# Kernel optimization log

Measured on AMD Instinct MI355X. Metric: run time of the kernel, lower is better.

Reference implementation:

```python
import jax, jax.numpy as jnp
import numpy as np

K = 16      # n_sample neighbors
L = 2       # stacked PT blocks
D = 128     # in_dim
H = 128     # hidden_dim = out_dim = vector_dim
EPS = 1e-5


def _bn(x, g, b, axes):
    # batch-norm with batch statistics (train-mode MinkowskiBatchNorm / BN1d / BN2d)
    m = jnp.mean(x, axes, keepdims=True)
    v = jnp.var(x, axes, keepdims=True)
    return (x - m) * jax.lax.rsqrt(v + EPS) * g + b


def setup_inputs():
    key = jax.random.key(0)
    ks = jax.random.split(key, 16)
    B, Nper = 2, 8192
    coords = jax.random.randint(ks[0], (B, Nper, 3), 0, 200, dtype=jnp.int32)
    feats = jax.random.normal(ks[1], (B * Nper, D), dtype=jnp.float32)
    w = lambda k, s: jax.random.normal(k, s, dtype=jnp.float32) * 0.1
    return {
        'coords': coords, 'feats': feats,
        'W_top': w(ks[2], (L, D, H)),
        'bn_top_g': jnp.ones((L, H)), 'bn_top_b': jnp.zeros((L, H)),
        'W_phi': w(ks[3], (L, H, H)),
        'W_psi': w(ks[4], (L, H, H)),
        'W_alpha': w(ks[5], (L, H, H)),
        'W_d1': w(ks[6], (L, 3, H)), 'b_d1': jnp.zeros((L, H)),
        'bn_d1_g': jnp.ones((L, H)), 'bn_d1_b': jnp.zeros((L, H)),
        'W_d2': w(ks[7], (L, H, H)), 'b_d2': jnp.zeros((L, H)),
        'bn_d2_g': jnp.ones((L, H)), 'bn_d2_b': jnp.zeros((L, H)),
        'W_g1': w(ks[8], (L, H, H)), 'b_g1': jnp.zeros((L, H)),
        'bn_g1_g': jnp.ones((L, H)), 'bn_g1_b': jnp.zeros((L, H)),
        'W_g2': w(ks[9], (L, H, H)), 'b_g2': jnp.zeros((L, H)),
        'bn_g2_g': jnp.ones((L, H)), 'bn_g2_b': jnp.zeros((L, H)),
        'W_down': w(ks[10], (L, H, D)),
        'bn_down_g': jnp.ones((L, D)), 'bn_down_b': jnp.zeros((L, D)),
    }


def _knn(coords):
    # cube_query with USE_KNN=True: per-scene KNN grouping (self included)
    cf = coords.astype(jnp.float32)

    def one(c):  # c: (Nper, 3)
        d2 = jnp.sum((c[:, None, :] - c[None, :, :]) ** 2, -1)  # (Nper, Nper)
        _, idx = jax.lax.top_k(-d2, K)
        return idx

    idx = jax.vmap(one)(cf)                      # (B, Nper, K) per-scene indices
    nbr = jax.vmap(lambda c, i: c[i])(cf, idx)   # (B, Nper, K, 3) grouped coords
    rel = nbr - cf[:, :, None, :]                # relative xyz (pose input)
    B, Nper = coords.shape[0], coords.shape[1]
    gidx = (idx + (jnp.arange(B, dtype=idx.dtype) * Nper)[:, None, None]).reshape(-1, K)
    return rel.reshape(-1, K, 3), gidx           # (N,K,3), (N,K) global indices


def reference(coords, feats, W_top, bn_top_g, bn_top_b, W_phi, W_psi, W_alpha,
              W_d1, b_d1, bn_d1_g, bn_d1_b, W_d2, b_d2, bn_d2_g, bn_d2_b,
              W_g1, b_g1, bn_g1_g, bn_g1_b, W_g2, b_g2, bn_g2_g, bn_g2_b,
              W_down, bn_down_g, bn_down_b):
    rel, gidx = _knn(coords)
    f = feats
    for l in range(L):
        h = _bn(f @ W_top[l], bn_top_g[l], bn_top_b[l], 0)  # linear_top (1x1 conv + BN)
        # delta: pointwise MLP 3 -> H -> H on relative xyz (position encoding)
        pose = jax.nn.relu(_bn(rel @ W_d1[l] + b_d1[l], bn_d1_g[l], bn_d1_b[l], (0, 1)))
        pose = _bn(pose @ W_d2[l] + b_d2[l], bn_d2_g[l], bn_d2_b[l], (0, 1))  # (N,K,H)
        q = h @ W_phi[l]               # (N, H)
        kk = (h @ W_psi[l])[gidx]      # neighbor keys   (N, K, H)
        v = (h @ W_alpha[l])[gidx]     # neighbor values (N, K, H)
        # gamma: pointwise MLP on (phi - psi + pose), vector attention logits
        a = q[:, None, :] - kk + pose
        a = jax.nn.relu(_bn(a @ W_g1[l] + b_g1[l], bn_g1_g[l], bn_g1_b[l], (0, 1)))
        a = _bn(a @ W_g2[l] + b_g2[l], bn_g2_g[l], bn_g2_b[l], (0, 1))
        attn = jax.nn.softmax(a, axis=1)          # per-channel softmax over K neighbors
        y = jnp.sum(attn * (v + pose), axis=1)    # (N, H) vector-attention aggregation
        y = _bn(y @ W_down[l], bn_down_g[l], bn_down_b[l], 0)  # linear_down + BN
        f = y + f                                  # residual
    return f
```

## Files before the change

kernel.cpp:

```cpp
#include <hip/hip_runtime.h>

using u16 = unsigned short;
using u32 = unsigned int;
using u64 = unsigned long long;

#define NPTS   16384
#define NPER   8192
#define KNN    16
#define NKROWS (NPTS*KNN)
#define HD     128
#define CAP    208
#define NSLOT  16

typedef _Float16 half8 __attribute__((ext_vector_type(8)));
typedef float    floatx4 __attribute__((ext_vector_type(4)));

__device__ __forceinline__ u16  f2h(float f){ _Float16 h=(_Float16)f; return __builtin_bit_cast(u16,h); }
__device__ __forceinline__ float h2f(u16 u){ return (float)__builtin_bit_cast(_Float16,u); }
__device__ __forceinline__ u32 umin32(u32 a,u32 b){ return a<b?a:b; }
__device__ __forceinline__ u32 mbcnt64(u64 m){
    return __builtin_amdgcn_mbcnt_hi((u32)(m>>32), __builtin_amdgcn_mbcnt_lo((u32)m,0));
}

__global__ __launch_bounds__(256) void pack_coords(const int* __restrict__ coords, u32* __restrict__ pc){
    int i = blockIdx.x*256 + threadIdx.x;
    pc[i] = (u32)coords[3*i] | ((u32)coords[3*i+1]<<8) | ((u32)coords[3*i+2]<<16);
}

struct WPtrs { const float* p[8]; };
__global__ __launch_bounds__(256) void prep_weights(WPtrs wp, u16* __restrict__ wt){
    int idx = blockIdx.x*256 + threadIdx.x;
    int t = idx>>15, rem = idx&32767;
    int l = rem>>14, e = rem&16383;
    int n = e>>7, k = e&127;
    wt[idx] = f2h(wp.p[t][l*16384 + k*128 + n]);
}

__global__ __launch_bounds__(512) void knn3(const u32* __restrict__ pc, int* __restrict__ idx_g,
                                            float* __restrict__ rel, u64* __restrict__ sM){
    __shared__ u32 sc[NPER];
    __shared__ u32 buf[8][CAP];
    __shared__ u64 red[9];
    int tid = threadIdx.x;
    int wave = tid>>6, lane = tid&63;
    int scene = blockIdx.x >> 10;
    int q = (blockIdx.x & 1023)*8 + wave;

    const uint4* s4 = (const uint4*)(pc + scene*NPER);
#pragma unroll
    for (int i=0;i<4;i++) ((uint4*)sc)[tid + i*512] = s4[tid + i*512];
    if (tid<9) red[tid]=0;
    if (lane<16) buf[wave][lane]=0xFFFFFFFFu;
    __syncthreads();

    u32 qp = sc[q];
    int qx=(int)(qp&255), qy=(int)((qp>>8)&255), qz=(int)((qp>>16)&255);
    u32 thresh = 0xFFFFFFFFu;
    u32 cnt = 16;

    auto tighten = [&](){
        u32 v0 = (lane      < (int)cnt) ? buf[wave][lane]      : 0xFFFFFFFFu;
        u32 v1 = (lane+64   < (int)cnt) ? buf[wave][lane+64]   : 0xFFFFFFFFu;
        u32 v2 = (lane+128  < (int)cnt) ? buf[wave][lane+128]  : 0xFFFFFFFFu;
        u32 v3 = (lane+192  < (int)cnt) ? buf[wave][lane+192]  : 0xFFFFFFFFu;
        u32 T = 0;
#pragma unroll
        for (int b=29;b>=0;b--){
            u32 Tt = T | (1u<<b);
            int c = __popcll(__ballot(v0<Tt)) + __popcll(__ballot(v1<Tt))
                  + __popcll(__ballot(v2<Tt)) + __popcll(__ballot(v3<Tt));
            if (c < 16) T = Tt;
        }
        u64 m0=__ballot(v0<=T), m1=__ballot(v1<=T), m2=__ballot(v2<=T), m3=__ballot(v3<=T);
        u32 b0=(u32)__popcll(m0), b1=(u32)__popcll(m1), b2=(u32)__popcll(m2);
        if (v0<=T) buf[wave][mbcnt64(m0)]=v0;
        if (v1<=T) buf[wave][b0+mbcnt64(m1)]=v1;
        if (v2<=T) buf[wave][b0+b1+mbcnt64(m2)]=v2;
        if (v3<=T) buf[wave][b0+b1+b2+mbcnt64(m3)]=v3;
        cnt = 16;
        thresh = T;
    };

    int lane2 = lane*2;
    uint2 p2 = ((const uint2*)sc)[lane];
    for (int t=0;t<64;t++){
        uint2 cur = p2;
        if (t<63) p2 = ((const uint2*)sc)[(t+1)*64+lane];
        int base = t*128 + lane2;
        u32 pa = cur.x;
        int dx0=(int)(pa&255)-qx, dy0=(int)((pa>>8)&255)-qy, dz0=(int)((pa>>16)&255)-qz;
        u32 d2_0 = (u32)(__mul24(dx0,dx0)+__mul24(dy0,dy0)+__mul24(dz0,dz0));
        u32 key0 = (d2_0<<13) + (u32)base;
        u32 pb = cur.y;
        int dx1=(int)(pb&255)-qx, dy1=(int)((pb>>8)&255)-qy, dz1=(int)((pb>>16)&255)-qz;
        u32 d2_1 = (u32)(__mul24(dx1,dx1)+__mul24(dy1,dy1)+__mul24(dz1,dz1));
        u32 key1 = (d2_1<<13) + (u32)(base+1);
        u64 m0 = __ballot(key0 < thresh);
        if (m0){
            u32 lt = mbcnt64(m0);
            if (key0 < thresh) buf[wave][cnt + lt] = key0;
            cnt += (u32)__popcll(m0);
            if (cnt > CAP-64) tighten();
        }
        u64 m1 = __ballot(key1 < thresh);
        if (m1){
            u32 lt = mbcnt64(m1);
            if (key1 < thresh) buf[wave][cnt + lt] = key1;
            cnt += (u32)__popcll(m1);
            if (cnt > CAP-64) tighten();
        }
    }
    tighten();

    {
        u32 myk = buf[wave][lane & 15];
        u32 rank = 0;
#pragma unroll
        for (int j=0;j<16;j++){ u32 o = buf[wave][j]; rank += (o < myk) ? 1u : 0u; }
        if (lane < 16) buf[wave][rank] = myk;
    }

    int n = scene*NPER + q;
    u32 key = buf[wave][lane & 15];
    int dx=0,dy=0,dz=0;
    if (lane<16){
        int j = (int)(key & 8191u);
        idx_g[(size_t)n*KNN + lane] = scene*NPER + j;
        u32 p = sc[j];
        dx=(int)(p&255)-qx; dy=(int)((p>>8)&255)-qy; dz=(int)((p>>16)&255)-qz;
        size_t ro = ((size_t)n*KNN+lane)*3;
        rel[ro]=(float)dx; rel[ro+1]=(float)dy; rel[ro+2]=(float)dz;
    }
    int arr[9] = {dx,dy,dz, dx*dx,dy*dy,dz*dz, dx*dy,dx*dz,dy*dz};
#pragma unroll
    for (int o=32;o>=1;o>>=1)
#pragma unroll
        for (int j=0;j<9;j++) arr[j] += __shfl_xor(arr[j], o, 64);
    if (lane==0)
#pragma unroll
        for (int j=0;j<9;j++) atomicAdd(&red[j], (u64)(long long)arr[j]);
    __syncthreads();
    if (tid<9) atomicAdd(&sM[tid], red[tid]);
}

__global__ __launch_bounds__(256) void finalize_d1(const u64* __restrict__ sM, const float* __restrict__ W_d1,
        const float* __restrict__ b_d1, const float* __restrict__ g, const float* __restrict__ beta,
        float* __restrict__ A, float* __restrict__ C){
    int tid=threadIdx.x; int l=tid>>7, c=tid&127;
    double s0=(double)(long long)sM[0], s1=(double)(long long)sM[1], s2=(double)(long long)sM[2];
    double m00=(double)(long long)sM[3], m11=(double)(long long)sM[4], m22=(double)(long long)sM[5];
    double m01=(double)(long long)sM[6], m02=(double)(long long)sM[7], m12=(double)(long long)sM[8];
    double w0=W_d1[l*384+c], w1=W_d1[l*384+128+c], w2=W_d1[l*384+256+c];
    double b =b_d1[l*128+c];
    double S = s0*w0+s1*w1+s2*w2;
    double Q = m00*w0*w0+m11*w1*w1+m22*w2*w2 + 2.0*(m01*w0*w1+m02*w0*w2+m12*w1*w2);
    double cnt = (double)NKROWS;
    double mean = S/cnt + b;
    double ex2  = (Q + 2.0*b*S)/cnt + b*b;
    double var  = ex2 - mean*mean;
    float a = g[l*128+c] * (float)(1.0/sqrt(var+1e-5));
    A[l*128+c]=a; C[l*128+c]=beta[l*128+c]-(float)mean*a;
}

__global__ void finalize_affine(double* __restrict__ P, const float* __restrict__ g,
        const float* __restrict__ b, double cnt, float* __restrict__ A, float* __restrict__ C){
    int c=threadIdx.x;
    double s=0.0, q=0.0;
#pragma unroll
    for (int k=0;k<NSLOT;k++){
        s+=P[k*256+c]; q+=P[k*256+128+c];
        P[k*256+c]=0.0; P[k*256+128+c]=0.0;
    }
    double mean=s/cnt, var=q/cnt-mean*mean;
    float a = g[c] * (float)(1.0/sqrt(var+1e-5));
    A[c]=a; C[c]=b[c]-(float)mean*a;
}

struct CompF32 {
    const float* src;
    __device__ __forceinline__ void stage(u16* As,int R0,int k0,int tid) const {
#pragma unroll
        for (int u=0;u<8;u++){
            int flat=u*256+tid, row=flat>>4, c4=flat&15; int k=k0+c4*4;
            const float4 v=*(const float4*)(src+(size_t)(R0+row)*HD+k);
            ushort4 o; o.x=f2h(v.x); o.y=f2h(v.y); o.z=f2h(v.z); o.w=f2h(v.w);
            *(ushort4*)(As+row*72+c4*4)=o;
        }
    }
};
struct CompH16Aff {
    const u16* src; const float* Aa; const float* Ca;
    __device__ __forceinline__ void stage(u16* As,int R0,int k0,int tid) const {
#pragma unroll
        for (int u=0;u<8;u++){
            int flat=u*256+tid, row=flat>>4, c4=flat&15; int k=k0+c4*4;
            const ushort4 v=*(const ushort4*)(src+(size_t)(R0+row)*HD+k);
            ushort4 o;
            o.x=f2h(h2f(v.x)*Aa[k]  +Ca[k]);   o.y=f2h(h2f(v.y)*Aa[k+1]+Ca[k+1]);
            o.z=f2h(h2f(v.z)*Aa[k+2]+Ca[k+2]); o.w=f2h(h2f(v.w)*Aa[k+3]+Ca[k+3]);
            *(ushort4*)(As+row*72+c4*4)=o;
        }
    }
};
struct CompH16AffRelu {
    const u16* src; const float* Aa; const float* Ca;
    __device__ __forceinline__ void stage(u16* As,int R0,int k0,int tid) const {
#pragma unroll
        for (int u=0;u<8;u++){
            int flat=u*256+tid, row=flat>>4, c4=flat&15; int k=k0+c4*4;
            const ushort4 v=*(const ushort4*)(src+(size_t)(R0+row)*HD+k);
            ushort4 o;
            o.x=f2h(fmaxf(h2f(v.x)*Aa[k]  +Ca[k],  0.f));
            o.y=f2h(fmaxf(h2f(v.y)*Aa[k+1]+Ca[k+1],0.f));
            o.z=f2h(fmaxf(h2f(v.z)*Aa[k+2]+Ca[k+2],0.f));
            o.w=f2h(fmaxf(h2f(v.w)*Aa[k+3]+Ca[k+3],0.f));
            *(ushort4*)(As+row*72+c4*4)=o;
        }
    }
};
struct CompPose1 {
    const float* rel; const float* Wd1; const float* bd1; const float* Aa; const float* Ca;
    __device__ __forceinline__ void stage(u16* As,int R0,int k0,int tid) const {
#pragma unroll
        for (int u=0;u<8;u++){
            int flat=u*256+tid, row=flat>>4, c4=flat&15; int k=k0+c4*4; int R=R0+row;
            float r0=rel[(size_t)R*3], r1=rel[(size_t)R*3+1], r2=rel[(size_t)R*3+2];
            ushort4 o;
#pragma unroll
            for (int j=0;j<4;j++){
                int kk=k+j;
                float x = r0*Wd1[kk] + r1*Wd1[HD+kk] + r2*Wd1[2*HD+kk] + bd1[kk];
                x = fmaxf(x*Aa[kk]+Ca[kk], 0.f);
                ((u16*)&o)[j]=f2h(x);
            }
            *(ushort4*)(As+row*72+c4*4)=o;
        }
    }
};
struct CompA0 {
    const u16* q; const u16* kp; const u16* pose; const int* gidx; const float* Aa; const float* Ca;
    __device__ __forceinline__ void stage(u16* As,int R0,int k0,int tid) const {
#pragma unroll
        for (int u=0;u<8;u++){
            int flat=u*256+tid, row=flat>>4, c4=flat&15; int k=k0+c4*4; int R=R0+row;
            int n=R>>4; int g=gidx[R];
            const ushort4 qv=*(const ushort4*)(q +(size_t)n*HD+k);
            const ushort4 kv=*(const ushort4*)(kp+(size_t)g*HD+k);
            const ushort4 pv=*(const ushort4*)(pose+(size_t)R*HD+k);
            ushort4 o;
            o.x=f2h(h2f(qv.x)-h2f(kv.x) + h2f(pv.x)*Aa[k]  +Ca[k]);
            o.y=f2h(h2f(qv.y)-h2f(kv.y) + h2f(pv.y)*Aa[k+1]+Ca[k+1]);
            o.z=f2h(h2f(qv.z)-h2f(kv.z) + h2f(pv.z)*Aa[k+2]+Ca[k+2]);
            o.w=f2h(h2f(qv.w)-h2f(kv.w) + h2f(pv.w)*Aa[k+3]+Ca[k+3]);
            *(ushort4*)(As+row*72+c4*4)=o;
        }
    }
};

template<class Comp, bool OUT16, bool HASBIAS, bool STATS>
__global__ __launch_bounds__(256) void gemm128(Comp comp, const u16* __restrict__ Wt,
        const float* __restrict__ bias, void* __restrict__ outp, double* __restrict__ statsP,
        int wtStride, long outStride){
    __shared__ __align__(16) u16 As[128*72];
    __shared__ __align__(16) u16 Bs[128*72];
    __shared__ float cs2[2][128], cq2[2][128];
    const u16* W = Wt + (size_t)blockIdx.y*wtStride;
    u16*   o16 = (u16*)outp   + (size_t)blockIdx.y*outStride;
    float* o32 = (float*)outp + (size_t)blockIdx.y*outStride;
    int tid=threadIdx.x;
    int R0=blockIdx.x*128;
    int lane=tid&63, wave=tid>>6, quad=lane>>4, r16=lane&15;
    int wm=wave>>1, wn=wave&1;
    floatx4 acc[4][4]={};
#pragma unroll
    for (int ks=0;ks<2;ks++){
        int k0=ks*64;
        comp.stage(As,R0,k0,tid);
#pragma unroll
        for (int u=0;u<4;u++){
            int flat=u*256+tid, n=flat>>3, c8=flat&7;
            *(int4*)(Bs+n*72+c8*8) = *(const int4*)(W+n*HD+k0+c8*8);
        }
        __syncthreads();
#pragma unroll
        for (int kk2=0;kk2<2;kk2++){
            half8 aF[4], bF[4];
#pragma unroll
            for (int mi=0;mi<4;mi++) aF[mi]=*(const half8*)(As+(wm*64+mi*16+r16)*72 + kk2*32+quad*8);
#pragma unroll
            for (int ni=0;ni<4;ni++) bF[ni]=*(const half8*)(Bs+(wn*64+ni*16+r16)*72 + kk2*32+quad*8);
#pragma unroll
            for (int mi=0;mi<4;mi++)
#pragma unroll
                for (int ni=0;ni<4;ni++)
                    acc[mi][ni]=__builtin_amdgcn_mfma_f32_16x16x32_f16(aF[mi],bF[ni],acc[mi][ni],0,0,0);
        }
        __syncthreads();
    }
    float sAcc[4]={0,0,0,0}, qAcc[4]={0,0,0,0};
#pragma unroll
    for (int mi=0;mi<4;mi++)
#pragma unroll
        for (int ni=0;ni<4;ni++){
            int col=wn*64+ni*16+r16;
            float bv = HASBIAS ? bias[col] : 0.f;
#pragma unroll
            for (int rg=0;rg<4;rg++){
                int row=R0+wm*64+mi*16+quad*4+rg;
                float v=acc[mi][ni][rg]+bv;
                if (STATS){ sAcc[ni]+=v; qAcc[ni]+=v*v; }
                if (OUT16) o16[(size_t)row*HD+col]=f2h(v);
                else       o32[(size_t)row*HD+col]=v;
            }
        }
    if (STATS){
#pragma unroll
        for (int ni=0;ni<4;ni++){
            float s=sAcc[ni], q=qAcc[ni];
            s += __shfl_xor(s,16,64); s += __shfl_xor(s,32,64);
            q += __shfl_xor(q,16,64); q += __shfl_xor(q,32,64);
            if (quad==0){
                int col=wn*64+ni*16+r16;
                cs2[wm][col]=s; cq2[wm][col]=q;
            }
        }
        __syncthreads();
        if (tid<128){
            int slot = blockIdx.x & (NSLOT-1);
            unsafeAtomicAdd(&statsP[slot*256+tid],     (double)(cs2[0][tid]+cs2[1][tid]));
            unsafeAtomicAdd(&statsP[slot*256+128+tid], (double)(cq2[0][tid]+cq2[1][tid]));
        }
    }
}

__global__ __launch_bounds__(256) void aggregate(const u16* __restrict__ a2, const u16* __restrict__ pose,
        const u16* __restrict__ vv, const int* __restrict__ gidx,
        const float* __restrict__ Ag2, const float* __restrict__ Cg2,
        const float* __restrict__ Ad2, const float* __restrict__ Cd2, float* __restrict__ y){
    int c=(threadIdx.x&63)*2, h=threadIdx.x>>6;
    int n=blockIdx.x*4+h;
    float sA0=Ag2[c], sC0=Cg2[c], pA0=Ad2[c], pC0=Cd2[c];
    float sA1=Ag2[c+1], sC1=Cg2[c+1], pA1=Ad2[c+1], pC1=Cd2[c+1];
    float av0[16], av1[16]; float m0=-1e30f, m1=-1e30f;
#pragma unroll
    for (int k=0;k<16;k++){
        ushort2 t=*(const ushort2*)(a2+((size_t)n*16+k)*HD+c);
        float a0=h2f(t.x)*sA0+sC0, a1=h2f(t.y)*sA1+sC1;
        av0[k]=a0; av1[k]=a1; m0=fmaxf(m0,a0); m1=fmaxf(m1,a1);
    }
    float sum0=0.f, sum1=0.f;
#pragma unroll
    for (int k=0;k<16;k++){
        float e0=__expf(av0[k]-m0), e1=__expf(av1[k]-m1);
        av0[k]=e0; av1[k]=e1; sum0+=e0; sum1+=e1;
    }
    float acc0=0.f, acc1=0.f;
#pragma unroll
    for (int k=0;k<16;k++){
        int g=gidx[n*16+k];
        ushort2 pt=*(const ushort2*)(pose+((size_t)n*16+k)*HD+c);
        ushort2 vt=*(const ushort2*)(vv+(size_t)g*HD+c);
        acc0 += av0[k]*(h2f(pt.x)*pA0+pC0 + h2f(vt.x));
        acc1 += av1[k]*(h2f(pt.y)*pA1+pC1 + h2f(vt.y));
    }
    y[(size_t)n*HD+c]  =acc0/sum0;
    y[(size_t)n*HD+c+1]=acc1/sum1;
}

__global__ __launch_bounds__(256) void residual(const float* __restrict__ ydown, const float* __restrict__ A,
        const float* __restrict__ C, const float* __restrict__ fin, float* __restrict__ fout){
    size_t i=(size_t)blockIdx.x*256+threadIdx.x; int c=(int)(i&127);
    fout[i]=ydown[i]*A[c]+C[c]+fin[i];
}

extern "C" void kernel_launch(void* const* d_in, const int* in_sizes, int n_in,
                              void* d_out, int out_size, void* d_ws, size_t ws_size,
                              hipStream_t stream){
    const int*   coords=(const int*)d_in[0];
    const float* feats=(const float*)d_in[1];
    const float* W_top=(const float*)d_in[2];
    const float* g_top=(const float*)d_in[3];
    const float* bt_top=(const float*)d_in[4];
    const float* W_phi=(const float*)d_in[5];
    const float* W_psi=(const float*)d_in[6];
    const float* W_alp=(const float*)d_in[7];
    const float* W_d1=(const float*)d_in[8];
    const float* b_d1=(const float*)d_in[9];
    const float* g_d1=(const float*)d_in[10];
    const float* bt_d1=(const float*)d_in[11];
    const float* W_d2=(const float*)d_in[12];
    const float* b_d2=(const float*)d_in[13];
    const float* g_d2=(const float*)d_in[14];
    const float* bt_d2=(const float*)d_in[15];
    const float* W_g1=(const float*)d_in[16];
    const float* b_g1=(const float*)d_in[17];
    const float* g_g1=(const float*)d_in[18];
    const float* bt_g1=(const float*)d_in[19];
    const float* W_g2=(const float*)d_in[20];
    const float* b_g2=(const float*)d_in[21];
    const float* g_g2=(const float*)d_in[22];
    const float* bt_g2=(const float*)d_in[23];
    const float* W_dn=(const float*)d_in[24];
    const float* g_dn=(const float*)d_in[25];
    const float* bt_dn=(const float*)d_in[26];

    char* ws=(char*)d_ws;
    size_t off=0;
    auto carve=[&](size_t bytes)->char*{ char* p=ws+off; off=(off+bytes+255)&~(size_t)255; return p; };
    u32*    pc    =(u32*)   carve((size_t)NPTS*4);
    int*    idxg  =(int*)   carve((size_t)NKROWS*4);
    float*  rel   =(float*) carve((size_t)NKROWS*3*4);
    u16*    h16   =(u16*)   carve((size_t)NPTS*HD*2);
    u16*    qb    =(u16*)   carve((size_t)3*NPTS*HD*2);
    u16*    kpb   = qb + (size_t)NPTS*HD;
    u16*    vvb   = qb + (size_t)2*NPTS*HD;
    float*  yb    =(float*) carve((size_t)NPTS*HD*4);
    float*  ydown =(float*) carve((size_t)NPTS*HD*4);
    float*  fbuf  =(float*) carve((size_t)NPTS*HD*4);
    u16*    wt    =(u16*)   carve((size_t)8*2*16384*2);
    char*   stats =         carve(NSLOT*256*8 + 256);
    double* P     =(double*)stats;
    u64*    sM    =(u64*)(stats + NSLOT*256*8);
    float*  aff   =(float*) carve(8192);
    float *A_top=aff, *C_top=aff+128, *A_d2=aff+256, *C_d2=aff+384,
          *A_g1=aff+512, *C_g1=aff+640, *A_g2=aff+768, *C_g2=aff+896,
          *A_dn=aff+1024, *C_dn=aff+1152, *A_d1=aff+1280, *C_d1=aff+1536;
    u16*    pose2 =(u16*)   carve((size_t)NKROWS*HD*2);
    u16*    abuf  =(u16*)   carve((size_t)NKROWS*HD*2);
    if (ws_size < off) return;

    hipMemsetAsync(stats, 0, NSLOT*256*8 + 256, stream);
    pack_coords<<<dim3(NPTS/256),dim3(256),0,stream>>>(coords, pc);
    WPtrs wp{{W_top,W_phi,W_psi,W_alp,W_d2,W_g1,W_g2,W_dn}};
    prep_weights<<<dim3(8*2*16384/256),dim3(256),0,stream>>>(wp, wt);
    knn3<<<dim3(2048),dim3(512),0,stream>>>(pc, idxg, rel, sM);
    finalize_d1<<<dim3(1),dim3(256),0,stream>>>(sM, W_d1, b_d1, g_d1, bt_d1, A_d1, C_d1);

    const float* fin=feats;
    for (int l=0;l<2;l++){
        const u16* wt_top=wt+(0*2+l)*16384; const u16* wt_phi=wt+(1*2+l)*16384;
        const u16* wt_d2 =wt+(4*2+l)*16384; const u16* wt_g1 =wt+(5*2+l)*16384;
        const u16* wt_g2 =wt+(6*2+l)*16384; const u16* wt_dn =wt+(7*2+l)*16384;

        gemm128<CompF32,true,false,true><<<dim3(NPTS/128),dim3(256),0,stream>>>(
            CompF32{fin}, wt_top, nullptr, h16, P, 0, 0);
        finalize_affine<<<dim3(1),dim3(128),0,stream>>>(P, g_top+l*128, bt_top+l*128, (double)NPTS, A_top, C_top);

        gemm128<CompH16Aff,true,false,false><<<dim3(NPTS/128,3),dim3(256),0,stream>>>(
            CompH16Aff{h16,A_top,C_top}, wt_phi, nullptr, qb, nullptr, 2*16384, (long)NPTS*HD);

        gemm128<CompPose1,true,true,true><<<dim3(NKROWS/128),dim3(256),0,stream>>>(
            CompPose1{rel, W_d1+l*384, b_d1+l*128, A_d1+l*128, C_d1+l*128}, wt_d2, b_d2+l*128, pose2, P, 0, 0);
        finalize_affine<<<dim3(1),dim3(128),0,stream>>>(P, g_d2+l*128, bt_d2+l*128, (double)NKROWS, A_d2, C_d2);

        gemm128<CompA0,true,true,true><<<dim3(NKROWS/128),dim3(256),0,stream>>>(
            CompA0{qb,kpb,pose2,idxg,A_d2,C_d2}, wt_g1, b_g1+l*128, abuf, P, 0, 0);
        finalize_affine<<<dim3(1),dim3(128),0,stream>>>(P, g_g1+l*128, bt_g1+l*128, (double)NKROWS, A_g1, C_g1);

        gemm128<CompH16AffRelu,true,true,true><<<dim3(NKROWS/128),dim3(256),0,stream>>>(
            CompH16AffRelu{abuf,A_g1,C_g1}, wt_g2, b_g2+l*128, abuf, P, 0, 0);
        finalize_affine<<<dim3(1),dim3(128),0,stream>>>(P, g_g2+l*128, bt_g2+l*128, (double)NKROWS, A_g2, C_g2);

        aggregate<<<dim3(NPTS/4),dim3(256),0,stream>>>(abuf, pose2, vvb, idxg, A_g2, C_g2, A_d2, C_d2, yb);

        gemm128<CompF32,false,false,true><<<dim3(NPTS/128),dim3(256),0,stream>>>(
            CompF32{yb}, wt_dn, nullptr, ydown, P, 0, 0);
        finalize_affine<<<dim3(1),dim3(128),0,stream>>>(P, g_dn+l*128, bt_dn+l*128, (double)NPTS, A_dn, C_dn);
        residual<<<dim3(NPTS*HD/256),dim3(256),0,stream>>>(ydown, A_dn, C_dn, fin, (l==1)?(float*)d_out:fbuf);
        fin=fbuf;
    }
}
```

Measured before the change: 527.9 us.

## Fuse BN finalize into consumer kernels and vectorize residual

Removes the separate single-block finalize_affine launches by having each consuming kernel (gemm, aggregate, residual) reduce the per-slot batch-norm partial sums into shared memory at block start. Stats buffers become separate regions per stage and layer so they no longer need zeroing between stages. The residual kernel now processes four floats per thread. The cost is redundant per-block reduction of 16 slots of doubles, traded against fewer launches and serialization points.

Result: no change. 521.7 us (-1.2%).

```diff
diff --git a/kernel.cpp b/kernel.cpp
--- a/kernel.cpp
+++ b/kernel.cpp
@@ -11,6 +11,7 @@
 #define HD     128
 #define CAP    208
 #define NSLOT  16
+#define NREG   10
 
 typedef _Float16 half8 __attribute__((ext_vector_type(8)));
 typedef float    floatx4 __attribute__((ext_vector_type(4)));
@@ -162,23 +163,20 @@
     A[l*128+c]=a; C[l*128+c]=beta[l*128+c]-(float)mean*a;
 }
 
-__global__ void finalize_affine(double* __restrict__ P, const float* __restrict__ g,
-        const float* __restrict__ b, double cnt, float* __restrict__ A, float* __restrict__ C){
-    int c=threadIdx.x;
+__device__ __forceinline__ void affine_reduce(const double* __restrict__ Pin,
+        const float* __restrict__ gin, const float* __restrict__ bin, double cntD,
+        float* Ash, float* Csh, int c){
     double s=0.0, q=0.0;
 #pragma unroll
-    for (int k=0;k<NSLOT;k++){
-        s+=P[k*256+c]; q+=P[k*256+128+c];
-        P[k*256+c]=0.0; P[k*256+128+c]=0.0;
-    }
-    double mean=s/cnt, var=q/cnt-mean*mean;
-    float a = g[c] * (float)(1.0/sqrt(var+1e-5));
-    A[c]=a; C[c]=b[c]-(float)mean*a;
+    for (int k=0;k<NSLOT;k++){ s+=Pin[k*256+c]; q+=Pin[k*256+128+c]; }
+    double mean=s/cntD, var=q/cntD-mean*mean;
+    float a = gin[c] * (float)(1.0/sqrt(var+1e-5));
+    Ash[c]=a; Csh[c]=bin[c]-(float)mean*a;
 }
 
 struct CompF32 {
     const float* src;
-    __device__ __forceinline__ void stage(u16* As,int R0,int k0,int tid) const {
+    __device__ __forceinline__ void stage(u16* As,int R0,int k0,int tid,const float*,const float*) const {
 #pragma unroll
         for (int u=0;u<8;u++){
             int flat=u*256+tid, row=flat>>4, c4=flat&15; int k=k0+c4*4;
@@ -189,8 +187,8 @@
     }
 };
 struct CompH16Aff {
-    const u16* src; const float* Aa; const float* Ca;
-    __device__ __forceinline__ void stage(u16* As,int R0,int k0,int tid) const {
+    const u16* src;
+    __device__ __forceinline__ void stage(u16* As,int R0,int k0,int tid,const float* Aa,const float* Ca) const {
 #pragma unroll
         for (int u=0;u<8;u++){
             int flat=u*256+tid, row=flat>>4, c4=flat&15; int k=k0+c4*4;
@@ -203,8 +201,8 @@
     }
 };
 struct CompH16AffRelu {
-    const u16* src; const float* Aa; const float* Ca;
-    __device__ __forceinline__ void stage(u16* As,int R0,int k0,int tid) const {
+    const u16* src;
+    __device__ __forceinline__ void stage(u16* As,int R0,int k0,int tid,const float* Aa,const float* Ca) const {
 #pragma unroll
         for (int u=0;u<8;u++){
             int flat=u*256+tid, row=flat>>4, c4=flat&15; int k=k0+c4*4;
@@ -220,7 +218,7 @@
 };
 struct CompPose1 {
     const float* rel; const float* Wd1; const float* bd1; const float* Aa; const float* Ca;
-    __device__ __forceinline__ void stage(u16* As,int R0,int k0,int tid) const {
+    __device__ __forceinline__ void stage(u16* As,int R0,int k0,int tid,const float*,const float*) const {
 #pragma unroll
         for (int u=0;u<8;u++){
             int flat=u*256+tid, row=flat>>4, c4=flat&15; int k=k0+c4*4; int R=R0+row;
@@ -238,8 +236,8 @@
     }
 };
 struct CompA0 {
-    const u16* q; const u16* kp; const u16* pose; const int* gidx; const float* Aa; const float* Ca;
-    __device__ __forceinline__ void stage(u16* As,int R0,int k0,int tid) const {
+    const u16* q; const u16* kp; const u16* pose; const int* gidx;
+    __device__ __forceinline__ void stage(u16* As,int R0,int k0,int tid,const float* Aa,const float* Ca) const {
 #pragma unroll
         for (int u=0;u<8;u++){
             int flat=u*256+tid, row=flat>>4, c4=flat&15; int k=k0+c4*4; int R=R0+row;
@@ -257,17 +255,24 @@
     }
 };
 
-template<class Comp, bool OUT16, bool HASBIAS, bool STATS>
+template<class Comp, bool OUT16, bool HASBIAS, bool STATS, bool AFF>
 __global__ __launch_bounds__(256) void gemm128(Comp comp, const u16* __restrict__ Wt,
         const float* __restrict__ bias, void* __restrict__ outp, double* __restrict__ statsP,
-        int wtStride, long outStride){
+        int wtStride, long outStride,
+        const double* __restrict__ Pin, const float* __restrict__ gin,
+        const float* __restrict__ bin, double cntD){
     __shared__ __align__(16) u16 As[128*72];
     __shared__ __align__(16) u16 Bs[128*72];
     __shared__ float cs2[2][128], cq2[2][128];
+    __shared__ float Aaff[128], Caff[128];
     const u16* W = Wt + (size_t)blockIdx.y*wtStride;
     u16*   o16 = (u16*)outp   + (size_t)blockIdx.y*outStride;
     float* o32 = (float*)outp + (size_t)blockIdx.y*outStride;
     int tid=threadIdx.x;
+    if (AFF){
+        if (tid<128) affine_reduce(Pin, gin, bin, cntD, Aaff, Caff, tid);
+        __syncthreads();
+    }
     int R0=blockIdx.x*128;
     int lane=tid&63, wave=tid>>6, quad=lane>>4, r16=lane&15;
     int wm=wave>>1, wn=wave&1;
@@ -275,7 +280,7 @@
 #pragma unroll
     for (int ks=0;ks<2;ks++){
         int k0=ks*64;
-        comp.stage(As,R0,k0,tid);
+        comp.stage(As,R0,k0,tid,Aaff,Caff);
 #pragma unroll
         for (int u=0;u<4;u++){
             int flat=u*256+tid, n=flat>>3, c8=flat&7;
@@ -335,17 +340,30 @@
 
 __global__ __launch_bounds__(256) void aggregate(const u16* __restrict__ a2, const u16* __restrict__ pose,
         const u16* __restrict__ vv, const int* __restrict__ gidx,
-        const float* __restrict__ Ag2, const float* __restrict__ Cg2,
-        const float* __restrict__ Ad2, const float* __restrict__ Cd2, float* __restrict__ y){
-    int c=(threadIdx.x&63)*2, h=threadIdx.x>>6;
+        const double* __restrict__ Pg2, const float* __restrict__ g_g2, const float* __restrict__ b_g2,
+        const double* __restrict__ Pd2, const float* __restrict__ g_d2, const float* __restrict__ b_d2,
+        float* __restrict__ y){
+    __shared__ float Ag2s[128], Cg2s[128], Ad2s[128], Cd2s[128];
+    int t=threadIdx.x;
+    {
+        int cc=t&127;
+        const double* Pp = (t<128)? Pg2 : Pd2;
+        const float*  gg = (t<128)? g_g2 : g_d2;
+        const float*  bb = (t<128)? b_g2 : b_d2;
+        float* Adst = (t<128)? Ag2s : Ad2s;
+        float* Cdst = (t<128)? Cg2s : Cd2s;
+        affine_reduce(Pp, gg, bb, (double)NKROWS, Adst, Cdst, cc);
+    }
+    __syncthreads();
+    int c=(t&63)*2, h=t>>6;
     int n=blockIdx.x*4+h;
-    float sA0=Ag2[c], sC0=Cg2[c], pA0=Ad2[c], pC0=Cd2[c];
-    float sA1=Ag2[c+1], sC1=Cg2[c+1], pA1=Ad2[c+1], pC1=Cd2[c+1];
+    float sA0=Ag2s[c], sC0=Cg2s[c], pA0=Ad2s[c], pC0=Cd2s[c];
+    float sA1=Ag2s[c+1], sC1=Cg2s[c+1], pA1=Ad2s[c+1], pC1=Cd2s[c+1];
     float av0[16], av1[16]; float m0=-1e30f, m1=-1e30f;
 #pragma unroll
     for (int k=0;k<16;k++){
-        ushort2 t=*(const ushort2*)(a2+((size_t)n*16+k)*HD+c);
-        float a0=h2f(t.x)*sA0+sC0, a1=h2f(t.y)*sA1+sC1;
+        ushort2 tt=*(const ushort2*)(a2+((size_t)n*16+k)*HD+c);
+        float a0=h2f(tt.x)*sA0+sC0, a1=h2f(tt.y)*sA1+sC1;
         av0[k]=a0; av1[k]=a1; m0=fmaxf(m0,a0); m1=fmaxf(m1,a1);
     }
     float sum0=0.f, sum1=0.f;
@@ -367,10 +385,22 @@
     y[(size_t)n*HD+c+1]=acc1/sum1;
 }
 
-__global__ __launch_bounds__(256) void residual(const float* __restrict__ ydown, const float* __restrict__ A,
-        const float* __restrict__ C, const float* __restrict__ fin, float* __restrict__ fout){
-    size_t i=(size_t)blockIdx.x*256+threadIdx.x; int c=(int)(i&127);
-    fout[i]=ydown[i]*A[c]+C[c]+fin[i];
+__global__ __launch_bounds__(256) void residual(const float* __restrict__ ydown,
+        const double* __restrict__ Pin, const float* __restrict__ gin, const float* __restrict__ bin,
+        const float* __restrict__ fin, float* __restrict__ fout){
+    __shared__ float Ash[128], Csh[128];
+    int tid=threadIdx.x;
+    if (tid<128) affine_reduce(Pin, gin, bin, (double)NPTS, Ash, Csh, tid);
+    __syncthreads();
+    size_t i=((size_t)blockIdx.x*256+tid)*4; int c=(int)(i&127);
+    float4 yv=*(const float4*)(ydown+i);
+    float4 fv=*(const float4*)(fin+i);
+    float4 o;
+    o.x=yv.x*Ash[c]  +Csh[c]  +fv.x;
+    o.y=yv.y*Ash[c+1]+Csh[c+1]+fv.y;
+    o.z=yv.z*Ash[c+2]+Csh[c+2]+fv.z;
+    o.w=yv.w*Ash[c+3]+Csh[c+3]+fv.w;
+    *(float4*)(fout+i)=o;
 }
 
 extern "C" void kernel_launch(void* const* d_in, const int* in_sizes, int n_in,
@@ -418,18 +448,18 @@
     float*  ydown =(float*) carve((size_t)NPTS*HD*4);
     float*  fbuf  =(float*) carve((size_t)NPTS*HD*4);
     u16*    wt    =(u16*)   carve((size_t)8*2*16384*2);
-    char*   stats =         carve(NSLOT*256*8 + 256);
+    char*   stats =         carve((size_t)NREG*NSLOT*256*8 + 256);
     double* P     =(double*)stats;
-    u64*    sM    =(u64*)(stats + NSLOT*256*8);
-    float*  aff   =(float*) carve(8192);
-    float *A_top=aff, *C_top=aff+128, *A_d2=aff+256, *C_d2=aff+384,
-          *A_g1=aff+512, *C_g1=aff+640, *A_g2=aff+768, *C_g2=aff+896,
-          *A_dn=aff+1024, *C_dn=aff+1152, *A_d1=aff+1280, *C_d1=aff+1536;
+    u64*    sM    =(u64*)(stats + (size_t)NREG*NSLOT*256*8);
+    float*  aff   =(float*) carve(4096);
+    float *A_d1=aff, *C_d1=aff+256;
     u16*    pose2 =(u16*)   carve((size_t)NKROWS*HD*2);
     u16*    abuf  =(u16*)   carve((size_t)NKROWS*HD*2);
     if (ws_size < off) return;
 
-    hipMemsetAsync(stats, 0, NSLOT*256*8 + 256, stream);
+    auto Preg=[&](int stage,int l)->double*{ return P + (size_t)(stage*2+l)*(NSLOT*256); };
+
+    hipMemsetAsync(stats, 0, (size_t)NREG*NSLOT*256*8 + 256, stream);
     pack_coords<<<dim3(NPTS/256),dim3(256),0,stream>>>(coords, pc);
     WPtrs wp{{W_top,W_phi,W_psi,W_alp,W_d2,W_g1,W_g2,W_dn}};
     prep_weights<<<dim3(8*2*16384/256),dim3(256),0,stream>>>(wp, wt);
@@ -442,31 +472,32 @@
         const u16* wt_d2 =wt+(4*2+l)*16384; const u16* wt_g1 =wt+(5*2+l)*16384;
         const u16* wt_g2 =wt+(6*2+l)*16384; const u16* wt_dn =wt+(7*2+l)*16384;
 
-        gemm128<CompF32,true,false,true><<<dim3(NPTS/128),dim3(256),0,stream>>>(
-            CompF32{fin}, wt_top, nullptr, h16, P, 0, 0);
-        finalize_affine<<<dim3(1),dim3(128),0,stream>>>(P, g_top+l*128, bt_top+l*128, (double)NPTS, A_top, C_top);
-
-        gemm128<CompH16Aff,true,false,false><<<dim3(NPTS/128,3),dim3(256),0,stream>>>(
-            CompH16Aff{h16,A_top,C_top}, wt_phi, nullptr, qb, nullptr, 2*16384, (long)NPTS*HD);
-
-        gemm128<CompPose1,true,true,true><<<dim3(NKROWS/128),dim3(256),0,stream>>>(
-            CompPose1{rel, W_d1+l*384, b_d1+l*128, A_d1+l*128, C_d1+l*128}, wt_d2, b_d2+l*128, pose2, P, 0, 0);
-        finalize_affine<<<dim3(1),dim3(128),0,stream>>>(P, g_d2+l*128, bt_d2+l*128, (double)NKROWS, A_d2, C_d2);
-
-        gemm128<CompA0,true,true,true><<<dim3(NKROWS/128),dim3(256),0,stream>>>(
-            CompA0{qb,kpb,pose2,idxg,A_d2,C_d2}, wt_g1, b_g1+l*128, abuf, P, 0, 0);
-        finalize_affine<<<dim3(1),dim3(128),0,stream>>>(P, g_g1+l*128, bt_g1+l*128, (double)NKROWS, A_g1, C_g1);
-
-        gemm128<CompH16AffRelu,true,true,true><<<dim3(NKROWS/128),dim3(256),0,stream>>>(
-            CompH16AffRelu{abuf,A_g1,C_g1}, wt_g2, b_g2+l*128, abuf, P, 0, 0);
-        finalize_affine<<<dim3(1),dim3(128),0,stream>>>(P, g_g2+l*128, bt_g2+l*128, (double)NKROWS, A_g2, C_g2);
-
-        aggregate<<<dim3(NPTS/4),dim3(256),0,stream>>>(abuf, pose2, vvb, idxg, A_g2, C_g2, A_d2, C_d2, yb);
-
-        gemm128<CompF32,false,false,true><<<dim3(NPTS/128),dim3(256),0,stream>>>(
-            CompF32{yb}, wt_dn, nullptr, ydown, P, 0, 0);
-        finalize_affine<<<dim3(1),dim3(128),0,stream>>>(P, g_dn+l*128, bt_dn+l*128, (double)NPTS, A_dn, C_dn);
-        residual<<<dim3(NPTS*HD/256),dim3(256),0,stream>>>(ydown, A_dn, C_dn, fin, (l==1)?(float*)d_out:fbuf);
+        gemm128<CompF32,true,false,true,false><<<dim3(NPTS/128),dim3(256),0,stream>>>(
+            CompF32{fin}, wt_top, nullptr, h16, Preg(0,l), 0, 0, nullptr, nullptr, nullptr, 0.0);
+
+        gemm128<CompH16Aff,true,false,false,true><<<dim3(NPTS/128,3),dim3(256),0,stream>>>(
+            CompH16Aff{h16}, wt_phi, nullptr, qb, nullptr, 2*16384, (long)NPTS*HD,
+            Preg(0,l), g_top+l*128, bt_top+l*128, (double)NPTS);
+
+        gemm128<CompPose1,true,true,true,false><<<dim3(NKROWS/128),dim3(256),0,stream>>>(
+            CompPose1{rel, W_d1+l*384, b_d1+l*128, A_d1+l*128, C_d1+l*128}, wt_d2, b_d2+l*128, pose2,
+            Preg(1,l), 0, 0, nullptr, nullptr, nullptr, 0.0);
+
+        gemm128<CompA0,true,true,true,true><<<dim3(NKROWS/128),dim3(256),0,stream>>>(
+            CompA0{qb,kpb,pose2,idxg}, wt_g1, b_g1+l*128, abuf, Preg(2,l), 0, 0,
+            Preg(1,l), g_d2+l*128, bt_d2+l*128, (double)NKROWS);
+
+        gemm128<CompH16AffRelu,true,true,true,true><<<dim3(NKROWS/128),dim3(256),0,stream>>>(
+            CompH16AffRelu{abuf}, wt_g2, b_g2+l*128, abuf, Preg(3,l), 0, 0,
+            Preg(2,l), g_g1+l*128, bt_g1+l*128, (double)NKROWS);
+
+        aggregate<<<dim3(NPTS/4),dim3(256),0,stream>>>(abuf, pose2, vvb, idxg,
+            Preg(3,l), g_g2+l*128, bt_g2+l*128, Preg(1,l), g_d2+l*128, bt_d2+l*128, yb);
+
+        gemm128<CompF32,false,false,true,false><<<dim3(NPTS/128),dim3(256),0,stream>>>(
+            CompF32{yb}, wt_dn, nullptr, ydown, Preg(4,l), 0, 0, nullptr, nullptr, nullptr, 0.0);
+        residual<<<dim3(NPTS*HD/1024),dim3(256),0,stream>>>(ydown,
+            Preg(4,l), g_dn+l*128, bt_dn+l*128, fin, (l==1)?(float*)d_out:fbuf);
         fin=fbuf;
     }
 }
```
